# Kernel tuning notes

Measured on AMD Instinct MI355X. Metric: run time of the kernel, lower is better.

The kernel has to match this reference:

```python
import jax, jax.numpy as jnp
import numpy as np

THRESHOLD = 0.5
NEG_RATIO = 3
ALPHA = 1.0
IMG_SIZE = 300.0  # convert_to_ratio divides pixel coords by image size


def _ssd300_default_boxes():
    """Canonical SSD300 priors: 8732 boxes in (cx, cy, w, h), clipped to [0,1]."""
    fmaps = [38, 19, 10, 5, 3, 1]
    scales = [0.1, 0.2, 0.375, 0.55, 0.725, 0.9]
    ars = [[1.0, 2.0, 0.5],
           [1.0, 2.0, 3.0, 0.5, 1.0 / 3.0],
           [1.0, 2.0, 3.0, 0.5, 1.0 / 3.0],
           [1.0, 2.0, 3.0, 0.5, 1.0 / 3.0],
           [1.0, 2.0, 0.5],
           [1.0, 2.0, 0.5]]
    boxes = []
    for k, (f, s) in enumerate(zip(fmaps, scales)):
        for i in range(f):
            for j in range(f):
                cx = (j + 0.5) / f
                cy = (i + 0.5) / f
                for ar in ars[k]:
                    boxes.append([cx, cy, s * np.sqrt(ar), s / np.sqrt(ar)])
                    if ar == 1.0:
                        s2 = np.sqrt(s * scales[k + 1]) if k < len(fmaps) - 1 else 1.0
                        boxes.append([cx, cy, s2, s2])
    return np.clip(np.asarray(boxes, dtype=np.float32), 0.0, 1.0)  # (8732, 4)


def _cxcy_to_xy(b):
    return jnp.concatenate([b[..., :2] - b[..., 2:] / 2.0,
                            b[..., :2] + b[..., 2:] / 2.0], axis=-1)


def _iou(a, b):
    # a: [N,4] xyxy, b: [P,4] xyxy -> [N,P]
    lt = jnp.maximum(a[:, None, :2], b[None, :, :2])
    rb = jnp.minimum(a[:, None, 2:], b[None, :, 2:])
    wh = jnp.clip(rb - lt, 0.0)
    inter = wh[..., 0] * wh[..., 1]
    area_a = (a[:, 2] - a[:, 0]) * (a[:, 3] - a[:, 1])
    area_b = (b[:, 2] - b[:, 0]) * (b[:, 3] - b[:, 1])
    return inter / (area_a[:, None] + area_b[None, :] - inter)


def _encode_cxcy(t, d):
    # standard SSD offsets (variances 0.1, 0.2). Safe log for unmatched (zero) boxes
    # -- those entries are masked out of the loss, matching torch's positive-only gather.
    g_cxcy = (t[..., :2] - d[..., :2]) / (d[..., 2:] / 10.0)
    safe_wh = jnp.where(t[..., 2:] > 0.0, t[..., 2:], d[..., 2:])
    g_wh = jnp.log(safe_wh / d[..., 2:]) * 5.0
    return jnp.concatenate([g_cxcy, g_wh], axis=-1)


def setup_inputs() -> dict:
    key = jax.random.key(0)
    k1, k2, k3, k4 = jax.random.split(key, 4)
    B, P, C, N = 128, 8732, 81, 16
    predicted_boxes = jax.random.normal(k1, (B, P, 4), dtype=jnp.float32)
    predicted_scores = jax.random.normal(k2, (B, P, C), dtype=jnp.float32)
    u = jax.random.uniform(k3, (B, N, 4), dtype=jnp.float32)
    cxcy = (0.15 + 0.7 * u[..., :2]) * IMG_SIZE   # centers in pixel coords
    wh = (0.08 + 0.32 * u[..., 2:]) * IMG_SIZE    # sizes in pixel coords
    target_boxes = jnp.concatenate([cxcy, wh], axis=-1)
    target_labels = jax.random.randint(k4, (B, N), 1, C)
    default_boxes = jnp.asarray(_ssd300_default_boxes())
    return {"predicted_boxes": predicted_boxes,
            "predicted_scores": predicted_scores,
            "target_boxes": target_boxes,
            "target_labels": target_labels,
            "default_boxes": default_boxes}


def reference(predicted_boxes, predicted_scores, target_boxes, target_labels, default_boxes):
    B, P, C = predicted_scores.shape
    db_xy = _cxcy_to_xy(default_boxes)
    tb = target_boxes / IMG_SIZE  # convert_to_ratio

    def match(boxes, labels):
        # boxes: [N,4] cxcywh (ratio), labels: [N]
        ov = _iou(_cxcy_to_xy(boxes), db_xy)          # [N, P]
        best_ov = ov.max(axis=0)                      # [P]
        obj_idx = ov.argmax(axis=0)                   # [P]
        box_idx = ov.argmax(axis=1)                   # [N] best prior per object
        obj_idx = obj_idx.at[box_idx].set(jnp.arange(boxes.shape[0]))
        check = best_ov > THRESHOLD                   # uses pre-scatter max (faithful)
        t_lab = jnp.where(check, labels[obj_idx], 0)
        t_box = jnp.where(check[:, None], boxes[obj_idx], 0.0)
        return _encode_cxcy(t_box, default_boxes), t_lab

    true_bboxes, true_labels = jax.vmap(match)(tb, target_labels)  # [B,P,4], [B,P]

    positive = true_labels != 0                        # [B,P]
    n_pos = jnp.maximum(positive.sum(), 1)

    # SmoothL1 (beta=1), mean over positive elements (num_pos * 4)
    diff = jnp.abs(predicted_boxes - true_bboxes)
    sl1 = jnp.where(diff < 1.0, 0.5 * diff * diff, diff - 0.5)
    bbox_loss = (sl1 * positive[..., None]).sum() / (n_pos.astype(sl1.dtype) * 4.0)

    # per-box cross entropy
    logp = jax.nn.log_softmax(predicted_scores, axis=-1)
    cls_all = -jnp.take_along_axis(logp, true_labels[..., None], axis=-1)[..., 0]  # [B,P]

    cls_pos_sum = (cls_all * positive).sum()
    neg = jnp.where(positive, 0.0, cls_all)
    neg_sorted = -jnp.sort(-neg, axis=1)               # descending per image
    n_hard = positive.sum(axis=1) * NEG_RATIO          # [B]
    rank = jnp.arange(P)[None, :]
    hard_neg_sum = (neg_sorted * (rank < n_hard[:, None])).sum()

    cls_loss = (cls_pos_sum + hard_neg_sum) / n_pos.astype(cls_all.dtype)
    return cls_loss + ALPHA * bbox_loss
```

## Files before the change

kernel.cpp:

```cpp
#include <hip/hip_runtime.h>
#include <hip/hip_bf16.h>
#include <math.h>

#define BB 128
#define PP 8732
#define NN 16
#define CC 81
#define IMG 300.0f
#define TILE_ROWS 64
#define NT ((BB * PP) / TILE_ROWS)
#define K1_THREADS 512

__global__ __launch_bounds__(K1_THREADS) void k1_match(
    const float* __restrict__ pred_boxes,
    const float* __restrict__ tgt_boxes,
    const int*   __restrict__ tgt_labels,
    const float* __restrict__ dboxes,
    int*   __restrict__ tlab_out,
    float* __restrict__ bbox_partial,
    int*   __restrict__ pos_count,
    int*   __restrict__ k3_done)
{
    const int b   = blockIdx.x;
    const int tid = threadIdx.x;
    const int NW  = K1_THREADS / 64;

    if (b == 0 && tid == 0) *k3_done = 0;

    __shared__ float t_cx[NN], t_cy[NN], t_w[NN], t_h[NN];
    __shared__ float t_x0s[NN], t_y0s[NN], t_x1s[NN], t_y1s[NN], t_areas[NN];
    __shared__ int   t_lab[NN];
    __shared__ unsigned char obj_s[PP];
    __shared__ unsigned char chk_s[PP];
    __shared__ float red_v[NN][NW];
    __shared__ int   red_i[NN][NW];
    __shared__ int   box_idx_s[NN];
    __shared__ float red_f[NW];
    __shared__ int   red_c[NW];

    if (tid < NN) {
        const float* tb = tgt_boxes + ((size_t)b * NN + tid) * 4;
        float cx = tb[0] / IMG, cy = tb[1] / IMG, w = tb[2] / IMG, h = tb[3] / IMG;
        t_cx[tid] = cx; t_cy[tid] = cy; t_w[tid] = w; t_h[tid] = h;
        float x0 = cx - w * 0.5f, y0 = cy - h * 0.5f;
        float x1 = cx + w * 0.5f, y1 = cy + h * 0.5f;
        t_x0s[tid] = x0; t_y0s[tid] = y0; t_x1s[tid] = x1; t_y1s[tid] = y1;
        t_areas[tid] = (x1 - x0) * (y1 - y0);
        t_lab[tid] = tgt_labels[(size_t)b * NN + tid];
    }
    __syncthreads();

    float tx0[NN], ty0[NN], tx1[NN], ty1[NN], tar[NN];
#pragma unroll
    for (int n = 0; n < NN; ++n) {
        tx0[n] = t_x0s[n]; ty0[n] = t_y0s[n];
        tx1[n] = t_x1s[n]; ty1[n] = t_y1s[n];
        tar[n] = t_areas[n];
    }

    float bestv[NN];
    int   bestp[NN];
#pragma unroll
    for (int n = 0; n < NN; ++n) { bestv[n] = -1.0f; bestp[n] = 0x7fffffff; }

    for (int p = tid; p < PP; p += K1_THREADS) {
        float4 d = *reinterpret_cast<const float4*>(dboxes + (size_t)p * 4);
        float dx0 = d.x - d.z * 0.5f, dy0 = d.y - d.w * 0.5f;
        float dx1 = d.x + d.z * 0.5f, dy1 = d.y + d.w * 0.5f;
        float dar = (dx1 - dx0) * (dy1 - dy0);

        float iou[NN];
#pragma unroll
        for (int n = 0; n < NN; ++n) {
            float lx = fmaxf(tx0[n], dx0);
            float ly = fmaxf(ty0[n], dy0);
            float rx = fminf(tx1[n], dx1);
            float ry = fminf(ty1[n], dy1);
            float iw = fmaxf(rx - lx, 0.0f);
            float ih = fmaxf(ry - ly, 0.0f);
            float inter = iw * ih;
            float den   = tar[n] + dar - inter;
            iou[n] = inter * __builtin_amdgcn_rcpf(den);
        }
        float bov = iou[0];
#pragma unroll
        for (int n = 1; n < NN; ++n) bov = fmaxf(bov, iou[n]);
        int bidx = 0;
#pragma unroll
        for (int n = NN - 1; n >= 0; --n) if (iou[n] == bov) bidx = n;
#pragma unroll
        for (int n = 0; n < NN; ++n) {
            if (iou[n] > bestv[n]) { bestv[n] = iou[n]; bestp[n] = p; }
        }
        obj_s[p] = (unsigned char)bidx;
        chk_s[p] = (bov > 0.5f) ? 1 : 0;
    }

#pragma unroll
    for (int n = 0; n < NN; ++n) {
        float v = bestv[n]; int ip = bestp[n];
        for (int off = 32; off; off >>= 1) {
            float v2 = __shfl_xor(v, off);
            int   p2 = __shfl_xor(ip, off);
            if (v2 > v || (v2 == v && p2 < ip)) { v = v2; ip = p2; }
        }
        if ((tid & 63) == 0) { red_v[n][tid >> 6] = v; red_i[n][tid >> 6] = ip; }
    }
    __syncthreads();
    if (tid < NN) {
        float v = red_v[tid][0]; int ip = red_i[tid][0];
        for (int w = 1; w < NW; ++w) {
            float v2 = red_v[tid][w]; int p2 = red_i[tid][w];
            if (v2 > v || (v2 == v && p2 < ip)) { v = v2; ip = p2; }
        }
        box_idx_s[tid] = ip;
    }
    __syncthreads();
    if (tid == 0) {
        for (int n = 0; n < NN; ++n) obj_s[box_idx_s[n]] = (unsigned char)n;
    }
    __syncthreads();

    float bacc = 0.0f;
    int   pcnt = 0;
    for (int p = tid; p < PP; p += K1_THREADS) {
        int lab = 0;
        if (chk_s[p]) {
            int n = obj_s[p];
            lab = t_lab[n];
            if (lab != 0) {
                ++pcnt;
                float4 d = *reinterpret_cast<const float4*>(dboxes + (size_t)p * 4);
                float gx = (t_cx[n] - d.x) / (d.z / 10.0f);
                float gy = (t_cy[n] - d.y) / (d.w / 10.0f);
                float gw = logf(t_w[n] / d.z) * 5.0f;
                float gh = logf(t_h[n] / d.w) * 5.0f;
                float4 pv = *reinterpret_cast<const float4*>(pred_boxes + ((size_t)b * PP + p) * 4);
                float dfs[4] = { pv.x - gx, pv.y - gy, pv.z - gw, pv.w - gh };
#pragma unroll
                for (int j = 0; j < 4; ++j) {
                    float ad = fabsf(dfs[j]);
                    bacc += (ad < 1.0f) ? 0.5f * ad * ad : ad - 0.5f;
                }
            }
        }
        tlab_out[(size_t)b * PP + p] = lab;
    }
    for (int off = 32; off; off >>= 1) {
        bacc += __shfl_xor(bacc, off);
        pcnt += __shfl_xor(pcnt, off);
    }
    if ((tid & 63) == 0) { red_f[tid >> 6] = bacc; red_c[tid >> 6] = pcnt; }
    __syncthreads();
    if (tid == 0) {
        float s = 0.0f; int c = 0;
        for (int w = 0; w < NW; ++w) { s += red_f[w]; c += red_c[w]; }
        bbox_partial[b] = s;
        pos_count[b]    = c;
    }
}

__global__ __launch_bounds__(256) void k2_cls(
    const float* __restrict__ scores,
    const int*   __restrict__ tlab,
    float* __restrict__ neg,
    float* __restrict__ clspos_partial)
{
    __shared__ float slds[TILE_ROWS * CC];
    const int tid = threadIdx.x;
    const int t   = blockIdx.x;

    const float* g = scores + (size_t)t * (TILE_ROWS * CC);
    for (int i = tid; i < TILE_ROWS * CC; i += 256)
        slds[i] = g[i];
    __syncthreads();

    const int row = tid >> 2;
    const int q   = tid & 3;
    const float* myrow = &slds[row * CC];
    const int base = q * 20;

    float x[21];
#pragma unroll
    for (int i = 0; i < 20; ++i) x[i] = myrow[base + i];
    x[20] = (q == 3) ? myrow[80] : -1e30f;

    float m = x[0];
#pragma unroll
    for (int i = 1; i < 21; ++i) m = fmaxf(m, x[i]);
    m = fmaxf(m, __shfl_xor(m, 1));
    m = fmaxf(m, __shfl_xor(m, 2));

    float s0 = 0.0f, s1 = 0.0f, s2 = 0.0f, s3 = 0.0f;
#pragma unroll
    for (int i = 0; i < 20; i += 4) {
        s0 += __expf(x[i + 0] - m);
        s1 += __expf(x[i + 1] - m);
        s2 += __expf(x[i + 2] - m);
        s3 += __expf(x[i + 3] - m);
    }
    s0 += __expf(x[20] - m);
    float s = (s0 + s1) + (s2 + s3);
    s += __shfl_xor(s, 1);
    s += __shfl_xor(s, 2);

    float acc = 0.0f;
    if (q == 0) {
        long long r = (long long)t * TILE_ROWS + row;
        int   lab = tlab[r];
        float cls = m + __logf(s) - slds[row * CC + lab];
        if (lab != 0) { acc = cls; neg[r] = 0.0f; }
        else          { neg[r] = cls; }
    }

    for (int off = 32; off; off >>= 1) acc += __shfl_xor(acc, off);
    __shared__ float wsum[4];
    if ((tid & 63) == 0) wsum[tid >> 6] = acc;
    __syncthreads();
    if (tid == 0)
        clspos_partial[t] = wsum[0] + wsum[1] + wsum[2] + wsum[3];
}

#define HREP 32
#define HPAD 257
#define CH   ((NT + BB - 1) / BB)
__global__ __launch_bounds__(256) void k3_topk_final(
    const float* __restrict__ neg,
    const int*   __restrict__ pos_count,
    const float* __restrict__ clspos_partial,
    const float* __restrict__ bbox_partial,
    float* __restrict__ hard_partial,
    float* __restrict__ clspos_red,
    int*   __restrict__ done,
    float* __restrict__ out)
{
    const int b    = blockIdx.x;
    const int tid  = threadIdx.x;
    const int lane = tid & 63;
    const int wv   = tid >> 6;
    const int rep  = lane >> 1;

    __shared__ unsigned int vals[PP];
    __shared__ int histR[HREP * HPAD];
    __shared__ int waveTot[4];
    __shared__ unsigned int s_prefix;
    __shared__ int s_kk;
    __shared__ float wsum[4];
    __shared__ float wsumc[4];
    __shared__ int s_last;

    for (int i = tid; i < PP; i += 256)
        vals[i] = __float_as_uint(neg[(size_t)b * PP + i]);

    {
        int start = b * CH;
        int end   = start + CH; if (end > NT) end = NT;
        float cv = (start + tid < end) ? clspos_partial[start + tid] : 0.0f;
        for (int off = 32; off; off >>= 1) cv += __shfl_xor(cv, off);
        if (lane == 0) wsumc[wv] = cv;
    }

    int k = pos_count[b] * 3;
    if (k > PP) k = PP;
    if (tid == 0) { s_prefix = 0u; s_kk = k; }
    __syncthreads();
    if (tid == 0)
        clspos_red[b] = wsumc[0] + wsumc[1] + wsumc[2] + wsumc[3];

    float hp = 0.0f;
    if (k > 0) {
        unsigned int prefmask = 0u;
        for (int round = 0; round < 4; ++round) {
            const int shift = 24 - 8 * round;
            for (int i = tid; i < HREP * HPAD; i += 256) histR[i] = 0;
            __syncthreads();
            const unsigned int pref = s_prefix;
            const int kkR = s_kk;
            for (int i = tid; i < PP; i += 256) {
                unsigned int v = vals[i];
                if ((v & prefmask) == pref)
                    atomicAdd(&histR[rep * HPAD + ((v >> shift) & 0xFF)], 1);
            }
            __syncthreads();
            int myh = 0;
#pragma unroll 8
            for (int r = 0; r < HREP; ++r) myh += histR[r * HPAD + tid];
            int s = myh;
#pragma unroll
            for (int off = 1; off < 64; off <<= 1) {
                int v = __shfl_down(s, off);
                if (lane + off < 64) s += v;
            }
            if (lane == 0) waveTot[wv] = s;
            __syncthreads();
            int addhi = 0;
            for (int w2 = wv + 1; w2 < 4; ++w2) addhi += waveTot[w2];
            s += addhi;
            int sg = s - myh;
            if (sg < kkR && sg + myh >= kkR) {
                s_prefix = pref | ((unsigned int)tid << shift);
                s_kk     = kkR - sg;
            }
            prefmask |= (0xFFu << shift);
        }
        __syncthreads();

        unsigned int t = s_prefix;
        int kk = s_kk;
        float tf = __uint_as_float(t);

        float acc = 0.0f;
        for (int i = tid; i < PP; i += 256) {
            unsigned int v = vals[i];
            if (v > t) acc += __uint_as_float(v);
        }
        for (int off = 32; off; off >>= 1) acc += __shfl_xor(acc, off);
        if (lane == 0) wsum[wv] = acc;
        __syncthreads();
        if (tid == 0)
            hp = wsum[0] + wsum[1] + wsum[2] + wsum[3] + (float)kk * tf;
    }
    if (tid == 0) hard_partial[b] = hp;

    __threadfence();
    if (tid == 0) s_last = (atomicAdd(done, 1) == BB - 1) ? 1 : 0;
    __syncthreads();
    if (!s_last) return;
    __threadfence();

    float cacc = 0.0f, bacc = 0.0f, hacc = 0.0f;
    int   pacc = 0;
    if (tid < BB) {
        cacc = clspos_red[tid];
        bacc = bbox_partial[tid];
        hacc = hard_partial[tid];
        pacc = pos_count[tid];
    }
    __shared__ float sc[256], sb[256], sh[256];
    __shared__ int   sp[256];
    sc[tid] = cacc; sb[tid] = bacc; sh[tid] = hacc; sp[tid] = pacc;
    __syncthreads();
    for (int off = 128; off; off >>= 1) {
        if (tid < off) {
            sc[tid] += sc[tid + off];
            sb[tid] += sb[tid + off];
            sh[tid] += sh[tid + off];
            sp[tid] += sp[tid + off];
        }
        __syncthreads();
    }
    if (tid == 0) {
        float npos = fmaxf((float)sp[0], 1.0f);
        out[0] = (sc[0] + sh[0]) / npos + sb[0] / (npos * 4.0f);
    }
}

extern "C" void kernel_launch(void* const* d_in, const int* in_sizes, int n_in,
                              void* d_out, int out_size, void* d_ws, size_t ws_size,
                              hipStream_t stream) {
    const float* pred_boxes  = (const float*)d_in[0];
    const float* pred_scores = (const float*)d_in[1];
    const float* tgt_boxes   = (const float*)d_in[2];
    const int*   tgt_labels  = (const int*)d_in[3];
    const float* dboxes      = (const float*)d_in[4];
    float* out = (float*)d_out;

    char* ws = (char*)d_ws;
    int*   tlab           = (int*)ws;   ws += (size_t)BB * PP * sizeof(int);
    float* neg            = (float*)ws; ws += (size_t)BB * PP * sizeof(float);
    int*   pos_count      = (int*)ws;   ws += BB * sizeof(int);
    float* bbox_partial   = (float*)ws; ws += BB * sizeof(float);
    float* hard_partial   = (float*)ws; ws += BB * sizeof(float);
    float* clspos_red     = (float*)ws; ws += BB * sizeof(float);
    int*   k3_done        = (int*)ws;   ws += 4 * sizeof(int);
    float* clspos_partial = (float*)ws; ws += (size_t)NT * sizeof(float);

    k1_match<<<BB, K1_THREADS, 0, stream>>>(pred_boxes, tgt_boxes, tgt_labels, dboxes,
                                            tlab, bbox_partial, pos_count, k3_done);
    k2_cls<<<NT, 256, 0, stream>>>(pred_scores, tlab, neg, clspos_partial);
    k3_topk_final<<<BB, 256, 0, stream>>>(neg, pos_count, clspos_partial,
                                          bbox_partial, hard_partial, clspos_red,
                                          k3_done, out);
}
```

Baseline: 139.9 us.

## Fuse matching and classification kernels with per-image ready flags

Merges the matching kernel and the per-row cross-entropy kernel into one launch. The first 128 blocks do matching and the remaining blocks compute log-softmax, then spin on a per-image flag published with release/acquire atomics before reading labels. This lets the bandwidth-heavy score loading and softmax overlap with the compute-bound matching, which previously used only 128 blocks. The matching block size drops from 512 to 256 threads. This relies on the low block indices being scheduled first to avoid deadlock, and it adds a memset launch and spin-wait overhead.

```diff
diff --git a/kernel.cpp b/kernel.cpp
--- a/kernel.cpp
+++ b/kernel.cpp
@@ -9,216 +9,238 @@
 #define IMG 300.0f
 #define TILE_ROWS 64
 #define NT ((BB * PP) / TILE_ROWS)
-#define K1_THREADS 512
-
-__global__ __launch_bounds__(K1_THREADS) void k1_match(
+#define NW1 4
+
+union SMem {
+    struct {
+        float t_cx[NN], t_cy[NN], t_w[NN], t_h[NN];
+        float t_x0s[NN], t_y0s[NN], t_x1s[NN], t_y1s[NN], t_areas[NN];
+        int   t_lab[NN];
+        unsigned char obj_s[PP];
+        unsigned char chk_s[PP];
+        float red_v[NN][NW1];
+        int   red_i[NN][NW1];
+        int   box_idx_s[NN];
+        float red_f[NW1];
+        int   red_c[NW1];
+    } a;
+    struct {
+        float slds[TILE_ROWS * CC];
+        float wsum[4];
+    } c;
+};
+
+__global__ __launch_bounds__(256) void k12_fused(
     const float* __restrict__ pred_boxes,
+    const float* __restrict__ pred_scores,
     const float* __restrict__ tgt_boxes,
     const int*   __restrict__ tgt_labels,
     const float* __restrict__ dboxes,
     int*   __restrict__ tlab_out,
     float* __restrict__ bbox_partial,
     int*   __restrict__ pos_count,
-    int*   __restrict__ k3_done)
+    float* __restrict__ neg,
+    float* __restrict__ clspos_partial,
+    int*   __restrict__ img_ready)
 {
-    const int b   = blockIdx.x;
+    __shared__ SMem sm;
     const int tid = threadIdx.x;
-    const int NW  = K1_THREADS / 64;
-
-    if (b == 0 && tid == 0) *k3_done = 0;
-
-    __shared__ float t_cx[NN], t_cy[NN], t_w[NN], t_h[NN];
-    __shared__ float t_x0s[NN], t_y0s[NN], t_x1s[NN], t_y1s[NN], t_areas[NN];
-    __shared__ int   t_lab[NN];
-    __shared__ unsigned char obj_s[PP];
-    __shared__ unsigned char chk_s[PP];
-    __shared__ float red_v[NN][NW];
-    __shared__ int   red_i[NN][NW];
-    __shared__ int   box_idx_s[NN];
-    __shared__ float red_f[NW];
-    __shared__ int   red_c[NW];
-
-    if (tid < NN) {
-        const float* tb = tgt_boxes + ((size_t)b * NN + tid) * 4;
-        float cx = tb[0] / IMG, cy = tb[1] / IMG, w = tb[2] / IMG, h = tb[3] / IMG;
-        t_cx[tid] = cx; t_cy[tid] = cy; t_w[tid] = w; t_h[tid] = h;
-        float x0 = cx - w * 0.5f, y0 = cy - h * 0.5f;
-        float x1 = cx + w * 0.5f, y1 = cy + h * 0.5f;
-        t_x0s[tid] = x0; t_y0s[tid] = y0; t_x1s[tid] = x1; t_y1s[tid] = y1;
-        t_areas[tid] = (x1 - x0) * (y1 - y0);
-        t_lab[tid] = tgt_labels[(size_t)b * NN + tid];
-    }
-    __syncthreads();
-
-    float tx0[NN], ty0[NN], tx1[NN], ty1[NN], tar[NN];
-#pragma unroll
-    for (int n = 0; n < NN; ++n) {
-        tx0[n] = t_x0s[n]; ty0[n] = t_y0s[n];
-        tx1[n] = t_x1s[n]; ty1[n] = t_y1s[n];
-        tar[n] = t_areas[n];
-    }
-
-    float bestv[NN];
-    int   bestp[NN];
-#pragma unroll
-    for (int n = 0; n < NN; ++n) { bestv[n] = -1.0f; bestp[n] = 0x7fffffff; }
-
-    for (int p = tid; p < PP; p += K1_THREADS) {
-        float4 d = *reinterpret_cast<const float4*>(dboxes + (size_t)p * 4);
-        float dx0 = d.x - d.z * 0.5f, dy0 = d.y - d.w * 0.5f;
-        float dx1 = d.x + d.z * 0.5f, dy1 = d.y + d.w * 0.5f;
-        float dar = (dx1 - dx0) * (dy1 - dy0);
-
-        float iou[NN];
+
+    if (blockIdx.x < BB) {
+        const int b = blockIdx.x;
+
+        if (tid < NN) {
+            const float* tb = tgt_boxes + ((size_t)b * NN + tid) * 4;
+            float cx = tb[0] / IMG, cy = tb[1] / IMG, w = tb[2] / IMG, h = tb[3] / IMG;
+            sm.a.t_cx[tid] = cx; sm.a.t_cy[tid] = cy; sm.a.t_w[tid] = w; sm.a.t_h[tid] = h;
+            float x0 = cx - w * 0.5f, y0 = cy - h * 0.5f;
+            float x1 = cx + w * 0.5f, y1 = cy + h * 0.5f;
+            sm.a.t_x0s[tid] = x0; sm.a.t_y0s[tid] = y0;
+            sm.a.t_x1s[tid] = x1; sm.a.t_y1s[tid] = y1;
+            sm.a.t_areas[tid] = (x1 - x0) * (y1 - y0);
+            sm.a.t_lab[tid] = tgt_labels[(size_t)b * NN + tid];
+        }
+        __syncthreads();
+
+        float tx0[NN], ty0[NN], tx1[NN], ty1[NN], tar[NN];
 #pragma unroll
         for (int n = 0; n < NN; ++n) {
-            float lx = fmaxf(tx0[n], dx0);
-            float ly = fmaxf(ty0[n], dy0);
-            float rx = fminf(tx1[n], dx1);
-            float ry = fminf(ty1[n], dy1);
-            float iw = fmaxf(rx - lx, 0.0f);
-            float ih = fmaxf(ry - ly, 0.0f);
-            float inter = iw * ih;
-            float den   = tar[n] + dar - inter;
-            iou[n] = inter * __builtin_amdgcn_rcpf(den);
-        }
-        float bov = iou[0];
-#pragma unroll
-        for (int n = 1; n < NN; ++n) bov = fmaxf(bov, iou[n]);
-        int bidx = 0;
-#pragma unroll
-        for (int n = NN - 1; n >= 0; --n) if (iou[n] == bov) bidx = n;
+            tx0[n] = sm.a.t_x0s[n]; ty0[n] = sm.a.t_y0s[n];
+            tx1[n] = sm.a.t_x1s[n]; ty1[n] = sm.a.t_y1s[n];
+            tar[n] = sm.a.t_areas[n];
+        }
+
+        float bestv[NN];
+        int   bestp[NN];
+#pragma unroll
+        for (int n = 0; n < NN; ++n) { bestv[n] = -1.0f; bestp[n] = 0x7fffffff; }
+
+        for (int p = tid; p < PP; p += 256) {
+            float4 d = *reinterpret_cast<const float4*>(dboxes + (size_t)p * 4);
+            float dx0 = d.x - d.z * 0.5f, dy0 = d.y - d.w * 0.5f;
+            float dx1 = d.x + d.z * 0.5f, dy1 = d.y + d.w * 0.5f;
+            float dar = (dx1 - dx0) * (dy1 - dy0);
+
+            float iou[NN];
+#pragma unroll
+            for (int n = 0; n < NN; ++n) {
+                float lx = fmaxf(tx0[n], dx0);
+                float ly = fmaxf(ty0[n], dy0);
+                float rx = fminf(tx1[n], dx1);
+                float ry = fminf(ty1[n], dy1);
+                float iw = fmaxf(rx - lx, 0.0f);
+                float ih = fmaxf(ry - ly, 0.0f);
+                float inter = iw * ih;
+                float den   = tar[n] + dar - inter;
+                iou[n] = inter * __builtin_amdgcn_rcpf(den);
+            }
+            float bov = iou[0];
+#pragma unroll
+            for (int n = 1; n < NN; ++n) bov = fmaxf(bov, iou[n]);
+            int bidx = 0;
+#pragma unroll
+            for (int n = NN - 1; n >= 0; --n) if (iou[n] == bov) bidx = n;
+#pragma unroll
+            for (int n = 0; n < NN; ++n) {
+                if (iou[n] > bestv[n]) { bestv[n] = iou[n]; bestp[n] = p; }
+            }
+            sm.a.obj_s[p] = (unsigned char)bidx;
+            sm.a.chk_s[p] = (bov > 0.5f) ? 1 : 0;
+        }
+
 #pragma unroll
         for (int n = 0; n < NN; ++n) {
-            if (iou[n] > bestv[n]) { bestv[n] = iou[n]; bestp[n] = p; }
-        }
-        obj_s[p] = (unsigned char)bidx;
-        chk_s[p] = (bov > 0.5f) ? 1 : 0;
-    }
-
-#pragma unroll
-    for (int n = 0; n < NN; ++n) {
-        float v = bestv[n]; int ip = bestp[n];
+            float v = bestv[n]; int ip = bestp[n];
+            for (int off = 32; off; off >>= 1) {
+                float v2 = __shfl_xor(v, off);
+                int   p2 = __shfl_xor(ip, off);
+                if (v2 > v || (v2 == v && p2 < ip)) { v = v2; ip = p2; }
+            }
+            if ((tid & 63) == 0) { sm.a.red_v[n][tid >> 6] = v; sm.a.red_i[n][tid >> 6] = ip; }
+        }
+        __syncthreads();
+        if (tid < NN) {
+            float v = sm.a.red_v[tid][0]; int ip = sm.a.red_i[tid][0];
+            for (int w = 1; w < NW1; ++w) {
+                float v2 = sm.a.red_v[tid][w]; int p2 = sm.a.red_i[tid][w];
+                if (v2 > v || (v2 == v && p2 < ip)) { v = v2; ip = p2; }
+            }
+            sm.a.box_idx_s[tid] = ip;
+        }
+        __syncthreads();
+        if (tid == 0) {
+            for (int n = 0; n < NN; ++n) sm.a.obj_s[sm.a.box_idx_s[n]] = (unsigned char)n;
+        }
+        __syncthreads();
+
+        float bacc = 0.0f;
+        int   pcnt = 0;
+        for (int p = tid; p < PP; p += 256) {
+            int lab = 0;
+            if (sm.a.chk_s[p]) {
+                int n = sm.a.obj_s[p];
+                lab = sm.a.t_lab[n];
+                if (lab != 0) {
+                    ++pcnt;
+                    float4 d = *reinterpret_cast<const float4*>(dboxes + (size_t)p * 4);
+                    float gx = (sm.a.t_cx[n] - d.x) / (d.z / 10.0f);
+                    float gy = (sm.a.t_cy[n] - d.y) / (d.w / 10.0f);
+                    float gw = logf(sm.a.t_w[n] / d.z) * 5.0f;
+                    float gh = logf(sm.a.t_h[n] / d.w) * 5.0f;
+                    float4 pv = *reinterpret_cast<const float4*>(pred_boxes + ((size_t)b * PP + p) * 4);
+                    float dfs[4] = { pv.x - gx, pv.y - gy, pv.z - gw, pv.w - gh };
+#pragma unroll
+                    for (int j = 0; j < 4; ++j) {
+                        float ad = fabsf(dfs[j]);
+                        bacc += (ad < 1.0f) ? 0.5f * ad * ad : ad - 0.5f;
+                    }
+                }
+            }
+            tlab_out[(size_t)b * PP + p] = lab;
+        }
         for (int off = 32; off; off >>= 1) {
-            float v2 = __shfl_xor(v, off);
-            int   p2 = __shfl_xor(ip, off);
-            if (v2 > v || (v2 == v && p2 < ip)) { v = v2; ip = p2; }
-        }
-        if ((tid & 63) == 0) { red_v[n][tid >> 6] = v; red_i[n][tid >> 6] = ip; }
-    }
-    __syncthreads();
-    if (tid < NN) {
-        float v = red_v[tid][0]; int ip = red_i[tid][0];
-        for (int w = 1; w < NW; ++w) {
-            float v2 = red_v[tid][w]; int p2 = red_i[tid][w];
-            if (v2 > v || (v2 == v && p2 < ip)) { v = v2; ip = p2; }
-        }
-        box_idx_s[tid] = ip;
-    }
-    __syncthreads();
-    if (tid == 0) {
-        for (int n = 0; n < NN; ++n) obj_s[box_idx_s[n]] = (unsigned char)n;
-    }
-    __syncthreads();
-
-    float bacc = 0.0f;
-    int   pcnt = 0;
-    for (int p = tid; p < PP; p += K1_THREADS) {
-        int lab = 0;
-        if (chk_s[p]) {
-            int n = obj_s[p];
-            lab = t_lab[n];
-            if (lab != 0) {
-                ++pcnt;
-                float4 d = *reinterpret_cast<const float4*>(dboxes + (size_t)p * 4);
-                float gx = (t_cx[n] - d.x) / (d.z / 10.0f);
-                float gy = (t_cy[n] - d.y) / (d.w / 10.0f);
-                float gw = logf(t_w[n] / d.z) * 5.0f;
-                float gh = logf(t_h[n] / d.w) * 5.0f;
-                float4 pv = *reinterpret_cast<const float4*>(pred_boxes + ((size_t)b * PP + p) * 4);
-                float dfs[4] = { pv.x - gx, pv.y - gy, pv.z - gw, pv.w - gh };
-#pragma unroll
-                for (int j = 0; j < 4; ++j) {
-                    float ad = fabsf(dfs[j]);
-                    bacc += (ad < 1.0f) ? 0.5f * ad * ad : ad - 0.5f;
-                }
-            }
-        }
-        tlab_out[(size_t)b * PP + p] = lab;
-    }
-    for (int off = 32; off; off >>= 1) {
-        bacc += __shfl_xor(bacc, off);
-        pcnt += __shfl_xor(pcnt, off);
-    }
-    if ((tid & 63) == 0) { red_f[tid >> 6] = bacc; red_c[tid >> 6] = pcnt; }
-    __syncthreads();
-    if (tid == 0) {
-        float s = 0.0f; int c = 0;
-        for (int w = 0; w < NW; ++w) { s += red_f[w]; c += red_c[w]; }
-        bbox_partial[b] = s;
-        pos_count[b]    = c;
-    }
-}
-
-__global__ __launch_bounds__(256) void k2_cls(
-    const float* __restrict__ scores,
-    const int*   __restrict__ tlab,
-    float* __restrict__ neg,
-    float* __restrict__ clspos_partial)
-{
-    __shared__ float slds[TILE_ROWS * CC];
-    const int tid = threadIdx.x;
-    const int t   = blockIdx.x;
-
-    const float* g = scores + (size_t)t * (TILE_ROWS * CC);
-    for (int i = tid; i < TILE_ROWS * CC; i += 256)
-        slds[i] = g[i];
-    __syncthreads();
-
-    const int row = tid >> 2;
-    const int q   = tid & 3;
-    const float* myrow = &slds[row * CC];
-    const int base = q * 20;
-
-    float x[21];
-#pragma unroll
-    for (int i = 0; i < 20; ++i) x[i] = myrow[base + i];
-    x[20] = (q == 3) ? myrow[80] : -1e30f;
-
-    float m = x[0];
-#pragma unroll
-    for (int i = 1; i < 21; ++i) m = fmaxf(m, x[i]);
-    m = fmaxf(m, __shfl_xor(m, 1));
-    m = fmaxf(m, __shfl_xor(m, 2));
-
-    float s0 = 0.0f, s1 = 0.0f, s2 = 0.0f, s3 = 0.0f;
-#pragma unroll
-    for (int i = 0; i < 20; i += 4) {
-        s0 += __expf(x[i + 0] - m);
-        s1 += __expf(x[i + 1] - m);
-        s2 += __expf(x[i + 2] - m);
-        s3 += __expf(x[i + 3] - m);
-    }
-    s0 += __expf(x[20] - m);
-    float s = (s0 + s1) + (s2 + s3);
-    s += __shfl_xor(s, 1);
-    s += __shfl_xor(s, 2);
-
-    float acc = 0.0f;
-    if (q == 0) {
-        long long r = (long long)t * TILE_ROWS + row;
-        int   lab = tlab[r];
-        float cls = m + __logf(s) - slds[row * CC + lab];
-        if (lab != 0) { acc = cls; neg[r] = 0.0f; }
-        else          { neg[r] = cls; }
-    }
-
-    for (int off = 32; off; off >>= 1) acc += __shfl_xor(acc, off);
-    __shared__ float wsum[4];
-    if ((tid & 63) == 0) wsum[tid >> 6] = acc;
-    __syncthreads();
-    if (tid == 0)
-        clspos_partial[t] = wsum[0] + wsum[1] + wsum[2] + wsum[3];
+            bacc += __shfl_xor(bacc, off);
+            pcnt += __shfl_xor(pcnt, off);
+        }
+        if ((tid & 63) == 0) { sm.a.red_f[tid >> 6] = bacc; sm.a.red_c[tid >> 6] = pcnt; }
+        __syncthreads();
+        if (tid == 0) {
+            float s = 0.0f; int c = 0;
+            for (int w = 0; w < NW1; ++w) { s += sm.a.red_f[w]; c += sm.a.red_c[w]; }
+            bbox_partial[b] = s;
+            pos_count[b]    = c;
+        }
+        __threadfence();
+        __syncthreads();
+        if (tid == 0)
+            __hip_atomic_store(&img_ready[b], 1, __ATOMIC_RELEASE,
+                               __HIP_MEMORY_SCOPE_AGENT);
+    } else {
+        const int t = blockIdx.x - BB;
+
+        const float* g = pred_scores + (size_t)t * (TILE_ROWS * CC);
+        for (int i = tid; i < TILE_ROWS * CC; i += 256)
+            sm.c.slds[i] = g[i];
+        __syncthreads();
+
+        const int row = tid >> 2;
+        const int q   = tid & 3;
+        const float* myrow = &sm.c.slds[row * CC];
+        const int base = q * 20;
+
+        float x[21];
+#pragma unroll
+        for (int i = 0; i < 20; ++i) x[i] = myrow[base + i];
+        x[20] = (q == 3) ? myrow[80] : -1e30f;
+
+        float m = x[0];
+#pragma unroll
+        for (int i = 1; i < 21; ++i) m = fmaxf(m, x[i]);
+        m = fmaxf(m, __shfl_xor(m, 1));
+        m = fmaxf(m, __shfl_xor(m, 2));
+
+        float s0 = 0.0f, s1 = 0.0f, s2 = 0.0f, s3 = 0.0f;
+#pragma unroll
+        for (int i = 0; i < 20; i += 4) {
+            s0 += __expf(x[i + 0] - m);
+            s1 += __expf(x[i + 1] - m);
+            s2 += __expf(x[i + 2] - m);
+            s3 += __expf(x[i + 3] - m);
+        }
+        s0 += __expf(x[20] - m);
+        float s = (s0 + s1) + (s2 + s3);
+        s += __shfl_xor(s, 1);
+        s += __shfl_xor(s, 2);
+
+        if (tid == 0) {
+            long long r0 = (long long)t * TILE_ROWS;
+            int img_lo = (int)(r0 / PP);
+            int img_hi = (int)((r0 + TILE_ROWS - 1) / PP);
+            while (__hip_atomic_load(&img_ready[img_lo], __ATOMIC_ACQUIRE,
+                                     __HIP_MEMORY_SCOPE_AGENT) == 0)
+                __builtin_amdgcn_s_sleep(2);
+            if (img_hi != img_lo)
+                while (__hip_atomic_load(&img_ready[img_hi], __ATOMIC_ACQUIRE,
+                                         __HIP_MEMORY_SCOPE_AGENT) == 0)
+                    __builtin_amdgcn_s_sleep(2);
+        }
+        __syncthreads();
+
+        float acc = 0.0f;
+        if (q == 0) {
+            long long r = (long long)t * TILE_ROWS + row;
+            int   lab = tlab_out[r];
+            float cls = m + __logf(s) - sm.c.slds[row * CC + lab];
+            if (lab != 0) { acc = cls; neg[r] = 0.0f; }
+            else          { neg[r] = cls; }
+        }
+
+        for (int off = 32; off; off >>= 1) acc += __shfl_xor(acc, off);
+        if ((tid & 63) == 0) sm.c.wsum[tid >> 6] = acc;
+        __syncthreads();
+        if (tid == 0)
+            clspos_partial[t] = sm.c.wsum[0] + sm.c.wsum[1] + sm.c.wsum[2] + sm.c.wsum[3];
+    }
 }
 
 #define HREP 32
@@ -373,11 +395,14 @@
     float* hard_partial   = (float*)ws; ws += BB * sizeof(float);
     float* clspos_red     = (float*)ws; ws += BB * sizeof(float);
     int*   k3_done        = (int*)ws;   ws += 4 * sizeof(int);
+    int*   img_ready      = (int*)ws;   ws += BB * sizeof(int);
     float* clspos_partial = (float*)ws; ws += (size_t)NT * sizeof(float);
 
-    k1_match<<<BB, K1_THREADS, 0, stream>>>(pred_boxes, tgt_boxes, tgt_labels, dboxes,
-                                            tlab, bbox_partial, pos_count, k3_done);
-    k2_cls<<<NT, 256, 0, stream>>>(pred_scores, tlab, neg, clspos_partial);
+    hipMemsetAsync(k3_done, 0, (4 + BB) * sizeof(int), stream);
+
+    k12_fused<<<BB + NT, 256, 0, stream>>>(pred_boxes, pred_scores, tgt_boxes,
+                                           tgt_labels, dboxes, tlab, bbox_partial,
+                                           pos_count, neg, clspos_partial, img_ready);
     k3_topk_final<<<BB, 256, 0, stream>>>(neg, pos_count, clspos_partial,
                                           bbox_partial, hard_partial, clspos_red,
                                           k3_done, out);
```

New measurement: 399.0 us. +185.2%, slower.

## Split per-image matching across two blocks with inter-block spin barrier

Applied to the files above, without the earlier changes.

The matching kernel now launches two blocks per image, each handling half of the priors, so 256 blocks run instead of 128 on a GPU with many CUs. The per-object best-prior argmax is exchanged through global memory using an atomic counter and spin-wait between the paired blocks. Partial bbox sums and positive counts are kept per half and combined in the final kernel, and counters are reset with a memset. The spin barrier assumes both blocks of a pair are co-resident, which holds for 256 blocks but adds a sync cost and a memset launch.

```diff
diff --git a/kernel.cpp b/kernel.cpp
--- a/kernel.cpp
+++ b/kernel.cpp
@@ -10,6 +10,8 @@
 #define TILE_ROWS 64
 #define NT ((BB * PP) / TILE_ROWS)
 #define K1_THREADS 512
+#define HALF_P (PP / 2)
+#define NW1 (K1_THREADS / 64)
 
 __global__ __launch_bounds__(K1_THREADS) void k1_match(
     const float* __restrict__ pred_boxes,
@@ -17,26 +19,27 @@
     const int*   __restrict__ tgt_labels,
     const float* __restrict__ dboxes,
     int*   __restrict__ tlab_out,
-    float* __restrict__ bbox_partial,
-    int*   __restrict__ pos_count,
-    int*   __restrict__ k3_done)
+    float* __restrict__ bbox_half,
+    int*   __restrict__ pos_half,
+    float* __restrict__ gv,
+    int*   __restrict__ gp,
+    int*   __restrict__ img_cnt)
 {
-    const int b   = blockIdx.x;
-    const int tid = threadIdx.x;
-    const int NW  = K1_THREADS / 64;
-
-    if (b == 0 && tid == 0) *k3_done = 0;
+    const int b    = blockIdx.x >> 1;
+    const int half = blockIdx.x & 1;
+    const int base = half * HALF_P;
+    const int tid  = threadIdx.x;
 
     __shared__ float t_cx[NN], t_cy[NN], t_w[NN], t_h[NN];
     __shared__ float t_x0s[NN], t_y0s[NN], t_x1s[NN], t_y1s[NN], t_areas[NN];
     __shared__ int   t_lab[NN];
-    __shared__ unsigned char obj_s[PP];
-    __shared__ unsigned char chk_s[PP];
-    __shared__ float red_v[NN][NW];
-    __shared__ int   red_i[NN][NW];
+    __shared__ unsigned char obj_s[HALF_P];
+    __shared__ unsigned char chk_s[HALF_P];
+    __shared__ float red_v[NN][NW1];
+    __shared__ int   red_i[NN][NW1];
     __shared__ int   box_idx_s[NN];
-    __shared__ float red_f[NW];
-    __shared__ int   red_c[NW];
+    __shared__ float red_f[NW1];
+    __shared__ int   red_c[NW1];
 
     if (tid < NN) {
         const float* tb = tgt_boxes + ((size_t)b * NN + tid) * 4;
@@ -63,7 +66,8 @@
 #pragma unroll
     for (int n = 0; n < NN; ++n) { bestv[n] = -1.0f; bestp[n] = 0x7fffffff; }
 
-    for (int p = tid; p < PP; p += K1_THREADS) {
+    for (int i = tid; i < HALF_P; i += K1_THREADS) {
+        const int p = base + i;
         float4 d = *reinterpret_cast<const float4*>(dboxes + (size_t)p * 4);
         float dx0 = d.x - d.z * 0.5f, dy0 = d.y - d.w * 0.5f;
         float dx1 = d.x + d.z * 0.5f, dy1 = d.y + d.w * 0.5f;
@@ -92,8 +96,8 @@
         for (int n = 0; n < NN; ++n) {
             if (iou[n] > bestv[n]) { bestv[n] = iou[n]; bestp[n] = p; }
         }
-        obj_s[p] = (unsigned char)bidx;
-        chk_s[p] = (bov > 0.5f) ? 1 : 0;
+        obj_s[i] = (unsigned char)bidx;
+        chk_s[i] = (bov > 0.5f) ? 1 : 0;
     }
 
 #pragma unroll
@@ -109,24 +113,49 @@
     __syncthreads();
     if (tid < NN) {
         float v = red_v[tid][0]; int ip = red_i[tid][0];
-        for (int w = 1; w < NW; ++w) {
+        for (int w = 1; w < NW1; ++w) {
             float v2 = red_v[tid][w]; int p2 = red_i[tid][w];
             if (v2 > v || (v2 == v && p2 < ip)) { v = v2; ip = p2; }
         }
-        box_idx_s[tid] = ip;
-    }
+        gv[blockIdx.x * NN + tid] = v;
+        gp[blockIdx.x * NN + tid] = ip;
+    }
+    __threadfence();
     __syncthreads();
     if (tid == 0) {
-        for (int n = 0; n < NN; ++n) obj_s[box_idx_s[n]] = (unsigned char)n;
+        __hip_atomic_fetch_add(&img_cnt[b], 1, __ATOMIC_RELEASE,
+                               __HIP_MEMORY_SCOPE_AGENT);
+        while (__hip_atomic_load(&img_cnt[b], __ATOMIC_ACQUIRE,
+                                 __HIP_MEMORY_SCOPE_AGENT) < 2)
+            __builtin_amdgcn_s_sleep(1);
+    }
+    __syncthreads();
+    __threadfence();
+
+    if (tid < NN) {
+        float v0 = gv[(b * 2 + 0) * NN + tid];
+        int   p0 = gp[(b * 2 + 0) * NN + tid];
+        float v1 = gv[(b * 2 + 1) * NN + tid];
+        int   p1 = gp[(b * 2 + 1) * NN + tid];
+        box_idx_s[tid] = (v1 > v0 || (v1 == v0 && p1 < p0)) ? p1 : p0;
+    }
+    __syncthreads();
+    if (tid == 0) {
+        for (int n = 0; n < NN; ++n) {
+            int bp = box_idx_s[n];
+            if (bp >= base && bp < base + HALF_P)
+                obj_s[bp - base] = (unsigned char)n;
+        }
     }
     __syncthreads();
 
     float bacc = 0.0f;
     int   pcnt = 0;
-    for (int p = tid; p < PP; p += K1_THREADS) {
+    for (int i = tid; i < HALF_P; i += K1_THREADS) {
+        const int p = base + i;
         int lab = 0;
-        if (chk_s[p]) {
-            int n = obj_s[p];
+        if (chk_s[i]) {
+            int n = obj_s[i];
             lab = t_lab[n];
             if (lab != 0) {
                 ++pcnt;
@@ -154,9 +183,9 @@
     __syncthreads();
     if (tid == 0) {
         float s = 0.0f; int c = 0;
-        for (int w = 0; w < NW; ++w) { s += red_f[w]; c += red_c[w]; }
-        bbox_partial[b] = s;
-        pos_count[b]    = c;
+        for (int w = 0; w < NW1; ++w) { s += red_f[w]; c += red_c[w]; }
+        bbox_half[blockIdx.x] = s;
+        pos_half[blockIdx.x]  = c;
     }
 }
 
@@ -226,9 +255,9 @@
 #define CH   ((NT + BB - 1) / BB)
 __global__ __launch_bounds__(256) void k3_topk_final(
     const float* __restrict__ neg,
-    const int*   __restrict__ pos_count,
+    const int*   __restrict__ pos_half,
     const float* __restrict__ clspos_partial,
-    const float* __restrict__ bbox_partial,
+    const float* __restrict__ bbox_half,
     float* __restrict__ hard_partial,
     float* __restrict__ clspos_red,
     int*   __restrict__ done,
@@ -260,7 +289,7 @@
         if (lane == 0) wsumc[wv] = cv;
     }
 
-    int k = pos_count[b] * 3;
+    int k = (pos_half[2 * b] + pos_half[2 * b + 1]) * 3;
     if (k > PP) k = PP;
     if (tid == 0) { s_prefix = 0u; s_kk = k; }
     __syncthreads();
@@ -328,16 +357,14 @@
     if (!s_last) return;
     __threadfence();
 
-    float cacc = 0.0f, bacc = 0.0f, hacc = 0.0f;
-    int   pacc = 0;
+    float cacc = 0.0f, bacc = 0.0f, hacc = 0.0f, pacc = 0.0f;
     if (tid < BB) {
         cacc = clspos_red[tid];
-        bacc = bbox_partial[tid];
         hacc = hard_partial[tid];
-        pacc = pos_count[tid];
-    }
-    __shared__ float sc[256], sb[256], sh[256];
-    __shared__ int   sp[256];
+    }
+    bacc = bbox_half[tid];
+    pacc = (float)pos_half[tid];
+    __shared__ float sc[256], sb[256], sh[256], sp[256];
     sc[tid] = cacc; sb[tid] = bacc; sh[tid] = hacc; sp[tid] = pacc;
     __syncthreads();
     for (int off = 128; off; off >>= 1) {
@@ -350,7 +377,7 @@
         __syncthreads();
     }
     if (tid == 0) {
-        float npos = fmaxf((float)sp[0], 1.0f);
+        float npos = fmaxf(sp[0], 1.0f);
         out[0] = (sc[0] + sh[0]) / npos + sb[0] / (npos * 4.0f);
     }
 }
@@ -368,17 +395,23 @@
     char* ws = (char*)d_ws;
     int*   tlab           = (int*)ws;   ws += (size_t)BB * PP * sizeof(int);
     float* neg            = (float*)ws; ws += (size_t)BB * PP * sizeof(float);
-    int*   pos_count      = (int*)ws;   ws += BB * sizeof(int);
-    float* bbox_partial   = (float*)ws; ws += BB * sizeof(float);
+    int*   k3_done        = (int*)ws;   ws += 4 * sizeof(int);
+    int*   img_cnt        = (int*)ws;   ws += BB * sizeof(int);
+    int*   pos_half       = (int*)ws;   ws += 2 * BB * sizeof(int);
+    float* bbox_half      = (float*)ws; ws += 2 * BB * sizeof(float);
     float* hard_partial   = (float*)ws; ws += BB * sizeof(float);
     float* clspos_red     = (float*)ws; ws += BB * sizeof(float);
-    int*   k3_done        = (int*)ws;   ws += 4 * sizeof(int);
+    float* gv             = (float*)ws; ws += 2 * BB * NN * sizeof(float);
+    int*   gp             = (int*)ws;   ws += 2 * BB * NN * sizeof(int);
     float* clspos_partial = (float*)ws; ws += (size_t)NT * sizeof(float);
 
-    k1_match<<<BB, K1_THREADS, 0, stream>>>(pred_boxes, tgt_boxes, tgt_labels, dboxes,
-                                            tlab, bbox_partial, pos_count, k3_done);
+    hipMemsetAsync(k3_done, 0, (4 + BB) * sizeof(int), stream);
+
+    k1_match<<<2 * BB, K1_THREADS, 0, stream>>>(pred_boxes, tgt_boxes, tgt_labels,
+                                                dboxes, tlab, bbox_half, pos_half,
+                                                gv, gp, img_cnt);
     k2_cls<<<NT, 256, 0, stream>>>(pred_scores, tlab, neg, clspos_partial);
-    k3_topk_final<<<BB, 256, 0, stream>>>(neg, pos_count, clspos_partial,
-                                          bbox_partial, hard_partial, clspos_red,
+    k3_topk_final<<<BB, 256, 0, stream>>>(neg, pos_half, clspos_partial,
+                                          bbox_half, hard_partial, clspos_red,
                                           k3_done, out);
 }
```

Result: slower. 197.4 us (+41.1%).
